# Kernel tuning notes

Measured on AMD Instinct MI355X. Metric: run time of the kernel, lower is better.

## Reference

```python
import jax, jax.numpy as jnp
import numpy as np
import math

N_HEADS = 12
EPS = 1e-5

def _layernorm(x, w, b):
    # torch .var() is unbiased (ddof=1)
    mean = jnp.mean(x, axis=-1, keepdims=True)
    var = jnp.var(x, axis=-1, keepdims=True, ddof=1)
    return (x - mean) / jnp.sqrt(var + EPS) * w + b

def _gelu_tanh(x):
    c = math.sqrt(2.0 / math.pi)
    return 0.5 * x * (1.0 + jnp.tanh(c * (x + 0.044715 * x * x * x)))

def setup_inputs() -> dict:
    key = jax.random.key(0)
    ks = jax.random.split(key, 6)
    B, T, C = 4, 2048, 768
    s = 0.02
    return {
        "x": jax.random.normal(ks[0], (B, T, C), jnp.float32),
        "ln1_w": jnp.ones((C,), jnp.float32),
        "ln1_b": jnp.zeros((C,), jnp.float32),
        "c_attn_w": jax.random.normal(ks[1], (C, 3 * C), jnp.float32) * s,
        "c_attn_b": jnp.zeros((3 * C,), jnp.float32),
        "c_proj_w": jax.random.normal(ks[2], (C, C), jnp.float32) * s,
        "c_proj_b": jnp.zeros((C,), jnp.float32),
        "ln2_w": jnp.ones((C,), jnp.float32),
        "ln2_b": jnp.zeros((C,), jnp.float32),
        "fc_w": jax.random.normal(ks[3], (C, 4 * C), jnp.float32) * s,
        "fc_b": jnp.zeros((4 * C,), jnp.float32),
        "mproj_w": jax.random.normal(ks[4], (4 * C, C), jnp.float32) * s,
        "mproj_b": jnp.zeros((C,), jnp.float32),
    }

def _attention(x, c_attn_w, c_attn_b, c_proj_w, c_proj_b):
    B, T, C = x.shape
    H = N_HEADS
    D = C // H
    qkv = x @ c_attn_w + c_attn_b  # [B,T,3C]
    q, k, v = jnp.split(qkv, 3, axis=-1)
    q = q.reshape(B, T, H, D).transpose(0, 2, 1, 3)  # [B,H,T,D]
    k = k.reshape(B, T, H, D).transpose(0, 2, 1, 3)
    v = v.reshape(B, T, H, D).transpose(0, 2, 1, 3)
    scores = jnp.einsum("bhqd,bhkd->bhqk", q, k) * (D ** -0.5)  # [B,H,T,T]
    causal = jnp.tril(jnp.ones((T, T), bool))
    scores = jnp.where(causal[None, None], scores, jnp.float32(-jnp.inf))
    attn = jax.nn.softmax(scores, axis=-1)
    out = jnp.einsum("bhqk,bhkd->bhqd", attn, v)  # [B,H,T,D]
    out = out.transpose(0, 2, 1, 3).reshape(B, T, C)
    return out @ c_proj_w + c_proj_b

def reference(x, ln1_w, ln1_b, c_attn_w, c_attn_b, c_proj_w, c_proj_b,
              ln2_w, ln2_b, fc_w, fc_b, mproj_w, mproj_b):
    x = x + _attention(_layernorm(x, ln1_w, ln1_b), c_attn_w, c_attn_b, c_proj_w, c_proj_b)
    h = _gelu_tanh(_layernorm(x, ln2_w, ln2_b) @ fc_w + fc_b)
    return x + h @ mproj_w + mproj_b
```

## Files before the change

### kernel.cpp

```cpp
#include <hip/hip_runtime.h>
#include <hip/hip_bf16.h>
#include <cstdint>

#define BF __hip_bfloat16

typedef __bf16 v8bf __attribute__((ext_vector_type(8)));
typedef float  v4f  __attribute__((ext_vector_type(4)));

__device__ __forceinline__ float tof(BF v) { return __bfloat162float(v); }
__device__ __forceinline__ BF    tob(float v) { return __float2bfloat16(v); }
__device__ __forceinline__ float ldf(float v) { return v; }
__device__ __forceinline__ float ldf(BF v) { return tof(v); }
__device__ __forceinline__ void stv(float* p, float v) { *p = v; }
__device__ __forceinline__ void stv(BF* p, float v) { *p = tob(v); }

__device__ __forceinline__ v4f mfma16(v8bf a, v8bf b, v4f c) {
  return __builtin_amdgcn_mfma_f32_16x16x32_bf16(a, b, c, 0, 0, 0);
}

__device__ __forceinline__ void async16(const BF* g, BF* l) {
  __builtin_amdgcn_global_load_lds((const __attribute__((address_space(1))) void*)g,
                                   (__attribute__((address_space(3))) void*)l, 16, 0, 0);
}

__global__ __launch_bounds__(256) void transpose_k(const float* __restrict__ in,
                                                   BF* __restrict__ out, int R, int C) {
  __shared__ BF t[64][65];
  int tid = threadIdx.x;
  int c0 = blockIdx.x * 64, r0 = blockIdx.y * 64;
#pragma unroll
  for (int i = 0; i < 16; ++i) {
    int idx = i * 256 + tid;
    int rr = idx >> 6, cc = idx & 63;
    t[rr][cc] = tob(in[(size_t)(r0 + rr) * C + c0 + cc]);
  }
  __syncthreads();
#pragma unroll
  for (int i = 0; i < 16; ++i) {
    int idx = i * 256 + tid;
    int rr = idx >> 6, cc = idx & 63;
    out[(size_t)(c0 + rr) * R + r0 + cc] = t[cc][rr];
  }
}

__global__ __launch_bounds__(256) void prep_k(
    const float* __restrict__ caw, BF* __restrict__ oca,
    const float* __restrict__ pw,  BF* __restrict__ opj,
    const float* __restrict__ fw,  BF* __restrict__ ofc,
    const float* __restrict__ mw,  BF* __restrict__ omp,
    const float* __restrict__ x, const float* __restrict__ lw,
    const float* __restrict__ lb, BF* __restrict__ y) {
  __shared__ BF t[64][65];
  __shared__ float rs[4][2];
  const int bid = blockIdx.x;
  const int tid = threadIdx.x;
  if (bid < 1728) {
    const float* in; BF* out; int R, C, bx, by;
    if (bid < 432)       { in = caw; out = oca; R = 768;  C = 2304; bx = bid % 36; by = bid / 36; }
    else if (bid < 576)  { int i = bid - 432;  in = pw; out = opj; R = 768;  C = 768;  bx = i % 12; by = i / 12; }
    else if (bid < 1152) { int i = bid - 576;  in = fw; out = ofc; R = 768;  C = 3072; bx = i % 48; by = i / 48; }
    else                 { int i = bid - 1152; in = mw; out = omp; R = 3072; C = 768;  bx = i % 12; by = i / 12; }
    int c0 = bx * 64, r0 = by * 64;
#pragma unroll
    for (int i = 0; i < 16; ++i) {
      int idx = i * 256 + tid;
      int rr = idx >> 6, cc = idx & 63;
      t[rr][cc] = tob(in[(size_t)(r0 + rr) * C + c0 + cc]);
    }
    __syncthreads();
#pragma unroll
    for (int i = 0; i < 16; ++i) {
      int idx = i * 256 + tid;
      int rr = idx >> 6, cc = idx & 63;
      out[(size_t)(c0 + rr) * R + r0 + cc] = t[cc][rr];
    }
  } else {
    int row = bid - 1728;
    const float* xr = x + (size_t)row * 768;
    float v0 = xr[tid], v1 = xr[tid + 256], v2 = xr[tid + 512];
    float s1 = v0 + v1 + v2;
    float s2 = v0 * v0 + v1 * v1 + v2 * v2;
#pragma unroll
    for (int m = 32; m; m >>= 1) { s1 += __shfl_xor(s1, m); s2 += __shfl_xor(s2, m); }
    int wv = tid >> 6;
    if ((tid & 63) == 0) { rs[wv][0] = s1; rs[wv][1] = s2; }
    __syncthreads();
    s1 = rs[0][0] + rs[1][0] + rs[2][0] + rs[3][0];
    s2 = rs[0][1] + rs[1][1] + rs[2][1] + rs[3][1];
    float mean = s1 * (1.0f / 768.0f);
    float var = fmaxf((s2 - s1 * mean) * (1.0f / 767.0f), 0.0f);
    float rstd = rsqrtf(var + 1e-5f);
    BF* yr = y + (size_t)row * 768;
    yr[tid]       = tob((v0 - mean) * rstd * lw[tid]       + lb[tid]);
    yr[tid + 256] = tob((v1 - mean) * rstd * lw[tid + 256] + lb[tid + 256]);
    yr[tid + 512] = tob((v2 - mean) * rstd * lw[tid + 512] + lb[tid + 512]);
  }
}

__global__ __launch_bounds__(256) void vtrans_k(const BF* __restrict__ qkv,
                                                BF* __restrict__ vT) {
  __shared__ BF t[64][65];
  int tid = threadIdx.x;
  int t0 = blockIdx.x * 64;
  int bh = blockIdx.y;
  int b = bh / 12, h = bh % 12;
  const BF* src = qkv + (size_t)(b * 2048 + t0) * 2304 + 1536 + h * 64;
#pragma unroll
  for (int i = 0; i < 16; ++i) {
    int idx = i * 256 + tid;
    int rr = idx >> 6, cc = idx & 63;
    t[rr][cc] = src[(size_t)rr * 2304 + cc];
  }
  __syncthreads();
  BF* dst = vT + (size_t)bh * 64 * 2048 + t0;
#pragma unroll
  for (int i = 0; i < 16; ++i) {
    int idx = i * 256 + tid;
    int rr = idx >> 6, cc = idx & 63;
    dst[(size_t)rr * 2048 + cc] = t[cc][rr];
  }
}

template <typename TX>
__global__ __launch_bounds__(256) void ln_k(const TX* __restrict__ x,
                                            const float* __restrict__ w,
                                            const float* __restrict__ bia,
                                            BF* __restrict__ y) {
  int row = blockIdx.x, tid = threadIdx.x;
  const TX* xr = x + (size_t)row * 768;
  float v0 = ldf(xr[tid]), v1 = ldf(xr[tid + 256]), v2 = ldf(xr[tid + 512]);
  float s1 = v0 + v1 + v2;
  float s2 = v0 * v0 + v1 * v1 + v2 * v2;
#pragma unroll
  for (int m = 32; m; m >>= 1) { s1 += __shfl_xor(s1, m); s2 += __shfl_xor(s2, m); }
  __shared__ float rs[4][2];
  int wv = tid >> 6;
  if ((tid & 63) == 0) { rs[wv][0] = s1; rs[wv][1] = s2; }
  __syncthreads();
  s1 = rs[0][0] + rs[1][0] + rs[2][0] + rs[3][0];
  s2 = rs[0][1] + rs[1][1] + rs[2][1] + rs[3][1];
  float mean = s1 * (1.0f / 768.0f);
  float var = fmaxf((s2 - s1 * mean) * (1.0f / 767.0f), 0.0f);
  float rstd = rsqrtf(var + 1e-5f);
  BF* yr = y + (size_t)row * 768;
  yr[tid]       = tob((v0 - mean) * rstd * w[tid]       + bia[tid]);
  yr[tid + 256] = tob((v1 - mean) * rstd * w[tid + 256] + bia[tid + 256]);
  yr[tid + 512] = tob((v2 - mean) * rstd * w[tid + 512] + bia[tid + 512]);
}

__device__ __forceinline__ float gelu_f(float x) {
  float u = 0.7978845608028654f * (x + 0.044715f * x * x * x);
  float e = exp2f(2.8853900817779268f * u);
  return 0.5f * x * (1.0f + (1.0f - 2.0f / (e + 1.0f)));
}

template <int BN, int ACT, bool RESID, typename TR, typename TO>
__global__ __launch_bounds__(256) void gemm_sm_k(
    const BF* __restrict__ A, const BF* __restrict__ Bt, const float* __restrict__ bias,
    const TR* __restrict__ resid, TO* __restrict__ out, int M, int N, int K) {
  constexpr int NW = BN / 32;
  __shared__ __align__(16) BF As[2][128 * 64];
  __shared__ __align__(16) BF Bs[2][BN * 64];
  const int tid = threadIdx.x;
  const int w = tid >> 6, lane = tid & 63;
  const int quad = lane >> 4, l16 = lane & 15;
  const int gx = gridDim.x;
  const int nwg = gx * gridDim.y;
  const int lid = blockIdx.y * gx + blockIdx.x;
  const int swz = (lid & 7) * (nwg >> 3) + (lid >> 3);
  const int m0 = (swz / gx) * 128, n0 = (swz % gx) * BN;
  const int wm = (w >> 1) * 64, wn = (w & 1) * (BN / 2);
  const int sr = lane >> 3;
  const int sc = ((lane & 7) ^ sr) * 8;

  v4f acc[4][NW];
#pragma unroll
  for (int i = 0; i < 4; ++i)
#pragma unroll
    for (int j = 0; j < NW; ++j) acc[i][j] = (v4f){0.f, 0.f, 0.f, 0.f};

  auto stage = [&](int bsel, int k0) {
#pragma unroll
    for (int i = 0; i < 4; ++i) {
      int r0 = w * 32 + i * 8;
      async16(A + (size_t)(m0 + r0 + sr) * K + k0 + sc, &As[bsel][r0 * 64]);
    }
    if (BN == 128) {
#pragma unroll
      for (int i = 0; i < 4; ++i) {
        int r0 = w * 32 + i * 8;
        async16(Bt + (size_t)(n0 + r0 + sr) * K + k0 + sc, &Bs[bsel][r0 * 64]);
      }
    } else {
#pragma unroll
      for (int i = 0; i < 2; ++i) {
        int r0 = w * 16 + i * 8;
        async16(Bt + (size_t)(n0 + r0 + sr) * K + k0 + sc, &Bs[bsel][r0 * 64]);
      }
    }
  };

  const int nkt = K >> 6;
  stage(0, 0);
  __syncthreads();
  for (int kt = 0; kt < nkt; ++kt) {
    const int cur = kt & 1;
    if (kt + 1 < nkt) stage(cur ^ 1, (kt + 1) << 6);
#pragma unroll
    for (int kk = 0; kk < 2; ++kk) {
      v8bf af[4], bfv[NW];
#pragma unroll
      for (int mi = 0; mi < 4; ++mi) {
        int row = wm + mi * 16 + l16;
        af[mi] = *(const v8bf*)&As[cur][row * 64 + (((kk * 4 + quad) ^ (row & 7)) * 8)];
      }
#pragma unroll
      for (int nj = 0; nj < NW; ++nj) {
        int row = wn + nj * 16 + l16;
        bfv[nj] = *(const v8bf*)&Bs[cur][row * 64 + (((kk * 4 + quad) ^ (row & 7)) * 8)];
      }
      __builtin_amdgcn_s_setprio(1);
#pragma unroll
      for (int mi = 0; mi < 4; ++mi)
#pragma unroll
        for (int nj = 0; nj < NW; ++nj)
          acc[mi][nj] = mfma16(af[mi], bfv[nj], acc[mi][nj]);
      __builtin_amdgcn_s_setprio(0);
    }
    __syncthreads();
  }

#pragma unroll
  for (int nj = 0; nj < NW; ++nj) {
    int col = n0 + wn + nj * 16 + l16;
    float bv = bias[col];
#pragma unroll
    for (int mi = 0; mi < 4; ++mi) {
      v4f c = acc[mi][nj];
#pragma unroll
      for (int r = 0; r < 4; ++r) {
        int row = m0 + wm + mi * 16 + quad * 4 + r;
        float v = c[r] + bv;
        if (RESID) v += ldf(resid[(size_t)row * N + col]);
        if (ACT == 1) v = gelu_f(v);
        stv(&out[(size_t)row * N + col], v);
      }
    }
  }
}

template <int ACT, bool RESID, typename TR, typename TO>
__global__ __launch_bounds__(256) void gemm3_k(
    const BF* __restrict__ A, const BF* __restrict__ Bt, const float* __restrict__ bias,
    const TR* __restrict__ resid, TO* __restrict__ out, int M, int N, int K) {
  __shared__ __align__(16) BF As[3][128 * 64];
  __shared__ __align__(16) BF Bs[3][64 * 64];
  const int tid = threadIdx.x;
  const int w = tid >> 6, lane = tid & 63;
  const int quad = lane >> 4, l16 = lane & 15;
  const int gx = gridDim.x;
  const int nwg = gx * gridDim.y;
  const int lid = blockIdx.y * gx + blockIdx.x;
  const int swz = (lid & 7) * (nwg >> 3) + (lid >> 3);
  const int m0 = (swz / gx) * 128, n0 = (swz % gx) * 64;
  const int wm = (w >> 1) * 64, wn = (w & 1) * 32;
  const int sr = lane >> 3;
  const int sc = ((lane & 7) ^ sr) * 8;

  v4f acc[4][2];
#pragma unroll
  for (int i = 0; i < 4; ++i)
#pragma unroll
    for (int j = 0; j < 2; ++j) acc[i][j] = (v4f){0.f, 0.f, 0.f, 0.f};

  auto stage = [&](int bsel, int kt) {
    const int k0 = kt << 6;
#pragma unroll
    for (int i = 0; i < 4; ++i) {
      int r0 = w * 32 + i * 8;
      async16(A + (size_t)(m0 + r0 + sr) * K + k0 + sc, &As[bsel][r0 * 64]);
    }
#pragma unroll
    for (int i = 0; i < 2; ++i) {
      int r0 = w * 16 + i * 8;
      async16(Bt + (size_t)(n0 + r0 + sr) * K + k0 + sc, &Bs[bsel][r0 * 64]);
    }
  };

  const int nkt = K >> 6;
  stage(0, 0);
  stage(1, 1);
  asm volatile("s_waitcnt vmcnt(6)" ::: "memory");
  __builtin_amdgcn_s_barrier();
  asm volatile("" ::: "memory");

  for (int kt = 0; kt < nkt; ++kt) {
    if (kt + 2 < nkt) stage((kt + 2) % 3, kt + 2);
    const BF* Ab = As[kt % 3];
    const BF* Bb = Bs[kt % 3];
#pragma unroll
    for (int kk = 0; kk < 2; ++kk) {
      v8bf af[4], bfv[2];
#pragma unroll
      for (int mi = 0; mi < 4; ++mi) {
        int row = wm + mi * 16 + l16;
        af[mi] = *(const v8bf*)&Ab[row * 64 + (((kk * 4 + quad) ^ (row & 7)) * 8)];
      }
#pragma unroll
      for (int nj = 0; nj < 2; ++nj) {
        int row = wn + nj * 16 + l16;
        bfv[nj] = *(const v8bf*)&Bb[row * 64 + (((kk * 4 + quad) ^ (row & 7)) * 8)];
      }
      __builtin_amdgcn_s_setprio(1);
#pragma unroll
      for (int mi = 0; mi < 4; ++mi)
#pragma unroll
        for (int nj = 0; nj < 2; ++nj)
          acc[mi][nj] = mfma16(af[mi], bfv[nj], acc[mi][nj]);
      __builtin_amdgcn_s_setprio(0);
    }
    if (kt + 1 < nkt) {
      if (kt + 2 < nkt) asm volatile("s_waitcnt vmcnt(6)" ::: "memory");
      else              asm volatile("s_waitcnt vmcnt(0)" ::: "memory");
      __builtin_amdgcn_s_barrier();
      asm volatile("" ::: "memory");
    }
  }

#pragma unroll
  for (int nj = 0; nj < 2; ++nj) {
    int col = n0 + wn + nj * 16 + l16;
    float bv = bias[col];
#pragma unroll
    for (int mi = 0; mi < 4; ++mi) {
      v4f c = acc[mi][nj];
#pragma unroll
      for (int r = 0; r < 4; ++r) {
        int row = m0 + wm + mi * 16 + quad * 4 + r;
        float v = c[r] + bv;
        if (RESID) v += ldf(resid[(size_t)row * N + col]);
        if (ACT == 1) v = gelu_f(v);
        stv(&out[(size_t)row * N + col], v);
      }
    }
  }
}

__global__ __launch_bounds__(256) void attn_k(const BF* __restrict__ qkv,
                                              const BF* __restrict__ vT,
                                              BF* __restrict__ out) {
  __shared__ __align__(16) BF Ks[64 * 64];
  __shared__ __align__(16) BF Vs[64 * 64];
  __shared__ __align__(16) BF Ps[4][16 * 64];
  const int tid = threadIdx.x;
  const int w = tid >> 6, lane = tid & 63;
  const int quad = lane >> 4, l16 = lane & 15;
  const int bid = blockIdx.x;
  const int qi = 31 - (bid / 48);
  const int bh = bid % 48;
  const int b = bh / 12, h = bh % 12;
  const int q0 = qi * 64;
  const int qf = q0 + w * 16;
  BF* Pw = &Ps[w][0];
  const float L2E = 1.4426950408889634f;

  auto sz = [](int r, int c) { return (r << 6) + (c ^ ((r & 7) << 3)); };

  const BF* qp = qkv + (size_t)(b * 2048 + qf + l16) * 2304 + h * 64;
  v8bf q0v = *(const v8bf*)(qp + quad * 8);
  v8bf q1v = *(const v8bf*)(qp + 32 + quad * 8);
#pragma unroll
  for (int i = 0; i < 8; ++i) {
    q0v[i] = (__bf16)(tof((BF)q0v[i]) * 0.125f);
    q1v[i] = (__bf16)(tof((BF)q1v[i]) * 0.125f);
  }
  v8bf ones;
#pragma unroll
  for (int i = 0; i < 8; ++i) ones[i] = (__bf16)1.0f;

  v4f O[4], S;
#pragma unroll
  for (int j = 0; j < 4; ++j) O[j] = (v4f){0.f, 0.f, 0.f, 0.f};
  S = (v4f){0.f, 0.f, 0.f, 0.f};

  const BF* kg = qkv + (size_t)b * 2048 * 2304 + 768 + h * 64;
  const BF* vg = vT + (size_t)bh * 64 * 2048;
  const int r0 = tid >> 3, c0 = (tid & 7) * 8;
  const int r1 = r0 + 32;
  const int nIter = qi + 1;

  v8bf nk0 = *(const v8bf*)(kg + (size_t)r0 * 2304 + c0);
  v8bf nk1 = *(const v8bf*)(kg + (size_t)r1 * 2304 + c0);
  v8bf nv0 = *(const v8bf*)(vg + (size_t)r0 * 2048 + c0);
  v8bf nv1 = *(const v8bf*)(vg + (size_t)r1 * 2048 + c0);

  for (int t = 0; t < nIter; ++t) {
    const int kt0 = t * 64;
    __syncthreads();
    *(v8bf*)&Ks[sz(r0, c0)] = nk0;
    *(v8bf*)&Ks[sz(r1, c0)] = nk1;
    *(v8bf*)&Vs[sz(r0, c0)] = nv0;
    *(v8bf*)&Vs[sz(r1, c0)] = nv1;
    __syncthreads();
    if (t + 1 < nIter) {
      const int kn = kt0 + 64;
      nk0 = *(const v8bf*)(kg + (size_t)(kn + r0) * 2304 + c0);
      nk1 = *(const v8bf*)(kg + (size_t)(kn + r1) * 2304 + c0);
      nv0 = *(const v8bf*)(vg + (size_t)r0 * 2048 + kn + c0);
      nv1 = *(const v8bf*)(vg + (size_t)r1 * 2048 + kn + c0);
    }
    v4f s[4];
    __builtin_amdgcn_s_setprio(1);
#pragma unroll
    for (int nt = 0; nt < 4; ++nt) {
      v8bf kf0 = *(const v8bf*)&Ks[sz(nt * 16 + l16, quad * 8)];
      v8bf kf1 = *(const v8bf*)&Ks[sz(nt * 16 + l16, 32 + quad * 8)];
      s[nt] = mfma16(q1v, kf1, mfma16(q0v, kf0, (v4f){0.f, 0.f, 0.f, 0.f}));
    }
    __builtin_amdgcn_s_setprio(0);
    if (t < qi) {
#pragma unroll
      for (int nt = 0; nt < 4; ++nt)
#pragma unroll
        for (int r = 0; r < 4; ++r)
          Pw[sz(quad * 4 + r, nt * 16 + l16)] = tob(exp2f(s[nt][r] * L2E));
    } else {
#pragma unroll
      for (int nt = 0; nt < 4; ++nt) {
        int key = kt0 + nt * 16 + l16;
#pragma unroll
        for (int r = 0; r < 4; ++r) {
          int qrow = qf + quad * 4 + r;
          float p = (key <= qrow) ? exp2f(s[nt][r] * L2E) : 0.f;
          Pw[sz(quad * 4 + r, nt * 16 + l16)] = tob(p);
        }
      }
    }
    asm volatile("s_waitcnt lgkmcnt(0)" ::: "memory");
    v8bf p0 = *(const v8bf*)&Pw[sz(l16, quad * 8)];
    v8bf p1 = *(const v8bf*)&Pw[sz(l16, 32 + quad * 8)];
    __builtin_amdgcn_s_setprio(1);
#pragma unroll
    for (int j = 0; j < 4; ++j) {
      v8bf vf0 = *(const v8bf*)&Vs[sz(j * 16 + l16, quad * 8)];
      v8bf vf1 = *(const v8bf*)&Vs[sz(j * 16 + l16, 32 + quad * 8)];
      O[j] = mfma16(p1, vf1, mfma16(p0, vf0, O[j]));
    }
    S = mfma16(p1, ones, mfma16(p0, ones, S));
    __builtin_amdgcn_s_setprio(0);
  }

#pragma unroll
  for (int r = 0; r < 4; ++r) {
    float inv = 1.0f / S[r];
    int row = b * 2048 + qf + quad * 4 + r;
    BF* op = out + (size_t)row * 768 + h * 64 + l16;
#pragma unroll
    for (int j = 0; j < 4; ++j) op[j * 16] = tob(O[j][r] * inv);
  }
}

extern "C" void kernel_launch(void* const* d_in, const int* in_sizes, int n_in,
                              void* d_out, int out_size, void* d_ws, size_t ws_size,
                              hipStream_t stream) {
  const float* x        = (const float*)d_in[0];
  const float* ln1_w    = (const float*)d_in[1];
  const float* ln1_b    = (const float*)d_in[2];
  const float* c_attn_w = (const float*)d_in[3];
  const float* c_attn_b = (const float*)d_in[4];
  const float* c_proj_w = (const float*)d_in[5];
  const float* c_proj_b = (const float*)d_in[6];
  const float* ln2_w    = (const float*)d_in[7];
  const float* ln2_b    = (const float*)d_in[8];
  const float* fc_w     = (const float*)d_in[9];
  const float* fc_b     = (const float*)d_in[10];
  const float* mproj_w  = (const float*)d_in[11];
  const float* mproj_b  = (const float*)d_in[12];
  float* out = (float*)d_out;
  char* wsb = (char*)d_ws;
  dim3 blk(256);

  BF* vT = (BF*)((char*)d_out + 12582912);

  const size_t NEED_BIG = 89653248;
  if (ws_size >= NEED_BIG) {
    BF* qkv      = (BF*)(wsb);
    BF* hbuf     = (BF*)(wsb);
    BF* x2       = (BF*)(wsb + 50331648);
    BF* wT_attn  = (BF*)(wsb + 62914560);
    BF* wT_proj  = (BF*)(wsb + 66453504);
    BF* wT_fc    = (BF*)(wsb + 67633152);
    BF* wT_mproj = (BF*)(wsb + 72351744);
    BF* lnbuf    = (BF*)(wsb + 77070336);
    BF* attnout  = (BF*)d_out;

    prep_k<<<dim3(9920), blk, 0, stream>>>(c_attn_w, wT_attn, c_proj_w, wT_proj,
                                           fc_w, wT_fc, mproj_w, wT_mproj,
                                           x, ln1_w, ln1_b, lnbuf);
    gemm3_k<0, false, float, BF><<<dim3(36, 64), blk, 0, stream>>>(
        lnbuf, wT_attn, c_attn_b, (const float*)nullptr, qkv, 8192, 2304, 768);
    vtrans_k<<<dim3(32, 48), blk, 0, stream>>>(qkv, vT);
    attn_k<<<dim3(1536), blk, 0, stream>>>(qkv, vT, attnout);
    gemm3_k<0, true, float, BF><<<dim3(12, 64), blk, 0, stream>>>(
        attnout, wT_proj, c_proj_b, x, x2, 8192, 768, 768);
    ln_k<BF><<<8192, blk, 0, stream>>>(x2, ln2_w, ln2_b, lnbuf);
    gemm_sm_k<128, 1, false, float, BF><<<dim3(24, 64), blk, 0, stream>>>(
        lnbuf, wT_fc, fc_b, (const float*)nullptr, hbuf, 8192, 3072, 768);
    gemm3_k<0, true, BF, float><<<dim3(12, 64), blk, 0, stream>>>(
        hbuf, wT_mproj, mproj_b, x2, out, 8192, 768, 3072);
  } else {
    BF* ws       = (BF*)d_ws;
    BF* qkv      = ws;
    BF* attnout  = ws + (size_t)18874368;
    BF* wT_attn  = attnout;
    BF* x2       = ws;
    BF* wT_proj  = ws + (size_t)6291456;
    BF* wT_fc    = ws + (size_t)6881280;
    BF* wT_mproj = ws + (size_t)9240576;
    BF* hbuf     = ws + (size_t)11599872;
    BF* lnbuf    = (BF*)d_out;

    transpose_k<<<dim3(36, 12), blk, 0, stream>>>(c_attn_w, wT_attn, 768, 2304);
    ln_k<float><<<8192, blk, 0, stream>>>(x, ln1_w, ln1_b, lnbuf);
    gemm3_k<0, false, float, BF><<<dim3(36, 64), blk, 0, stream>>>(
        lnbuf, wT_attn, c_attn_b, (const float*)nullptr, qkv, 8192, 2304, 768);
    vtrans_k<<<dim3(32, 48), blk, 0, stream>>>(qkv, vT);
    attn_k<<<dim3(1536), blk, 0, stream>>>(qkv, vT, attnout);
    transpose_k<<<dim3(12, 12), blk, 0, stream>>>(c_proj_w, wT_proj, 768, 768);
    gemm3_k<0, true, float, BF><<<dim3(12, 64), blk, 0, stream>>>(
        attnout, wT_proj, c_proj_b, x, x2, 8192, 768, 768);
    ln_k<BF><<<8192, blk, 0, stream>>>(x2, ln2_w, ln2_b, lnbuf);
    transpose_k<<<dim3(48, 12), blk, 0, stream>>>(fc_w, wT_fc, 768, 3072);
    transpose_k<<<dim3(12, 48), blk, 0, stream>>>(mproj_w, wT_mproj, 3072, 768);
    for (int half = 1; half >= 0; --half) {
      size_t r0 = (size_t)half * 4096;
      gemm_sm_k<128, 1, false, float, BF><<<dim3(24, 32), blk, 0, stream>>>(
          lnbuf + r0 * 768, wT_fc, fc_b, (const float*)nullptr, hbuf, 4096, 3072, 768);
      gemm3_k<0, true, BF, float><<<dim3(12, 32), blk, 0, stream>>>(
          hbuf, wT_mproj, mproj_b, x2 + r0 * 768, out + r0 * 768, 4096, 768, 3072);
    }
  }
}
```

Measured before the change: 416.1 us.

## Replace triple-buffered GEMM with 64x128 double-buffered tile and revert to gemm_sm_k

Converts the 128x64 triple-buffered gemm3_k into a 64x128 double-buffered gemm64_k that synchronises with plain __syncthreads, and uses it for the FC GEMM. The QKV, attention-projection and MLP-projection GEMMs go back to the older gemm_sm_k variants with different tile widths. The aim is to trade tile shapes and pipelining depth per GEMM for better occupancy or wave count. The cost is a shallower prefetch pipeline and heavier barrier sync in the new kernel, which could expose global-load latency.

After: 359.7 us. -13.5%, faster.

```diff
diff --git a/kernel.cpp b/kernel.cpp
--- a/kernel.cpp
+++ b/kernel.cpp
@@ -250,11 +250,11 @@
 }
 
 template <int ACT, bool RESID, typename TR, typename TO>
-__global__ __launch_bounds__(256) void gemm3_k(
+__global__ __launch_bounds__(256) void gemm64_k(
     const BF* __restrict__ A, const BF* __restrict__ Bt, const float* __restrict__ bias,
     const TR* __restrict__ resid, TO* __restrict__ out, int M, int N, int K) {
-  __shared__ __align__(16) BF As[3][128 * 64];
-  __shared__ __align__(16) BF Bs[3][64 * 64];
+  __shared__ __align__(16) BF As[2][64 * 64];
+  __shared__ __align__(16) BF Bs[2][128 * 64];
   const int tid = threadIdx.x;
   const int w = tid >> 6, lane = tid & 63;
   const int quad = lane >> 4, l16 = lane & 15;
@@ -262,77 +262,66 @@
   const int nwg = gx * gridDim.y;
   const int lid = blockIdx.y * gx + blockIdx.x;
   const int swz = (lid & 7) * (nwg >> 3) + (lid >> 3);
-  const int m0 = (swz / gx) * 128, n0 = (swz % gx) * 64;
-  const int wm = (w >> 1) * 64, wn = (w & 1) * 32;
+  const int m0 = (swz / gx) * 64, n0 = (swz % gx) * 128;
+  const int wm = (w >> 1) * 32, wn = (w & 1) * 64;
   const int sr = lane >> 3;
   const int sc = ((lane & 7) ^ sr) * 8;
 
-  v4f acc[4][2];
-#pragma unroll
-  for (int i = 0; i < 4; ++i)
-#pragma unroll
-    for (int j = 0; j < 2; ++j) acc[i][j] = (v4f){0.f, 0.f, 0.f, 0.f};
-
-  auto stage = [&](int bsel, int kt) {
-    const int k0 = kt << 6;
+  v4f acc[2][4];
+#pragma unroll
+  for (int i = 0; i < 2; ++i)
+#pragma unroll
+    for (int j = 0; j < 4; ++j) acc[i][j] = (v4f){0.f, 0.f, 0.f, 0.f};
+
+  auto stage = [&](int bsel, int k0) {
+#pragma unroll
+    for (int i = 0; i < 2; ++i) {
+      int r0 = w * 16 + i * 8;
+      async16(A + (size_t)(m0 + r0 + sr) * K + k0 + sc, &As[bsel][r0 * 64]);
+    }
 #pragma unroll
     for (int i = 0; i < 4; ++i) {
       int r0 = w * 32 + i * 8;
-      async16(A + (size_t)(m0 + r0 + sr) * K + k0 + sc, &As[bsel][r0 * 64]);
-    }
-#pragma unroll
-    for (int i = 0; i < 2; ++i) {
-      int r0 = w * 16 + i * 8;
       async16(Bt + (size_t)(n0 + r0 + sr) * K + k0 + sc, &Bs[bsel][r0 * 64]);
     }
   };
 
   const int nkt = K >> 6;
   stage(0, 0);
-  stage(1, 1);
-  asm volatile("s_waitcnt vmcnt(6)" ::: "memory");
-  __builtin_amdgcn_s_barrier();
-  asm volatile("" ::: "memory");
-
+  __syncthreads();
   for (int kt = 0; kt < nkt; ++kt) {
-    if (kt + 2 < nkt) stage((kt + 2) % 3, kt + 2);
-    const BF* Ab = As[kt % 3];
-    const BF* Bb = Bs[kt % 3];
+    const int cur = kt & 1;
+    if (kt + 1 < nkt) stage(cur ^ 1, (kt + 1) << 6);
 #pragma unroll
     for (int kk = 0; kk < 2; ++kk) {
-      v8bf af[4], bfv[2];
-#pragma unroll
-      for (int mi = 0; mi < 4; ++mi) {
+      v8bf af[2], bfv[4];
+#pragma unroll
+      for (int mi = 0; mi < 2; ++mi) {
         int row = wm + mi * 16 + l16;
-        af[mi] = *(const v8bf*)&Ab[row * 64 + (((kk * 4 + quad) ^ (row & 7)) * 8)];
-      }
-#pragma unroll
-      for (int nj = 0; nj < 2; ++nj) {
+        af[mi] = *(const v8bf*)&As[cur][row * 64 + (((kk * 4 + quad) ^ (row & 7)) * 8)];
+      }
+#pragma unroll
+      for (int nj = 0; nj < 4; ++nj) {
         int row = wn + nj * 16 + l16;
-        bfv[nj] = *(const v8bf*)&Bb[row * 64 + (((kk * 4 + quad) ^ (row & 7)) * 8)];
+        bfv[nj] = *(const v8bf*)&Bs[cur][row * 64 + (((kk * 4 + quad) ^ (row & 7)) * 8)];
       }
       __builtin_amdgcn_s_setprio(1);
 #pragma unroll
-      for (int mi = 0; mi < 4; ++mi)
-#pragma unroll
-        for (int nj = 0; nj < 2; ++nj)
+      for (int mi = 0; mi < 2; ++mi)
+#pragma unroll
+        for (int nj = 0; nj < 4; ++nj)
           acc[mi][nj] = mfma16(af[mi], bfv[nj], acc[mi][nj]);
       __builtin_amdgcn_s_setprio(0);
     }
-    if (kt + 1 < nkt) {
-      if (kt + 2 < nkt) asm volatile("s_waitcnt vmcnt(6)" ::: "memory");
-      else              asm volatile("s_waitcnt vmcnt(0)" ::: "memory");
-      __builtin_amdgcn_s_barrier();
-      asm volatile("" ::: "memory");
-    }
-  }
-
-#pragma unroll
-  for (int nj = 0; nj < 2; ++nj) {
+    __syncthreads();
+  }
+
+#pragma unroll
+  for (int nj = 0; nj < 4; ++nj) {
     int col = n0 + wn + nj * 16 + l16;
     float bv = bias[col];
 #pragma unroll
-    for (int mi = 0; mi < 4; ++mi) {
+    for (int mi = 0; mi < 2; ++mi) {
       v4f c = acc[mi][nj];
 #pragma unroll
       for (int r = 0; r < 4; ++r) {
@@ -497,16 +486,16 @@
     prep_k<<<dim3(9920), blk, 0, stream>>>(c_attn_w, wT_attn, c_proj_w, wT_proj,
                                            fc_w, wT_fc, mproj_w, wT_mproj,
                                            x, ln1_w, ln1_b, lnbuf);
-    gemm3_k<0, false, float, BF><<<dim3(36, 64), blk, 0, stream>>>(
+    gemm_sm_k<128, 0, false, float, BF><<<dim3(18, 64), blk, 0, stream>>>(
         lnbuf, wT_attn, c_attn_b, (const float*)nullptr, qkv, 8192, 2304, 768);
     vtrans_k<<<dim3(32, 48), blk, 0, stream>>>(qkv, vT);
     attn_k<<<dim3(1536), blk, 0, stream>>>(qkv, vT, attnout);
-    gemm3_k<0, true, float, BF><<<dim3(12, 64), blk, 0, stream>>>(
+    gemm_sm_k<64, 0, true, float, BF><<<dim3(12, 64), blk, 0, stream>>>(
         attnout, wT_proj, c_proj_b, x, x2, 8192, 768, 768);
     ln_k<BF><<<8192, blk, 0, stream>>>(x2, ln2_w, ln2_b, lnbuf);
-    gemm_sm_k<128, 1, false, float, BF><<<dim3(24, 64), blk, 0, stream>>>(
+    gemm64_k<1, false, float, BF><<<dim3(24, 128), blk, 0, stream>>>(
         lnbuf, wT_fc, fc_b, (const float*)nullptr, hbuf, 8192, 3072, 768);
-    gemm3_k<0, true, BF, float><<<dim3(12, 64), blk, 0, stream>>>(
+    gemm_sm_k<64, 0, true, BF, float><<<dim3(12, 64), blk, 0, stream>>>(
         hbuf, wT_mproj, mproj_b, x2, out, 8192, 768, 3072);
   } else {
     BF* ws       = (BF*)d_ws;
@@ -522,12 +511,12 @@
 
     transpose_k<<<dim3(36, 12), blk, 0, stream>>>(c_attn_w, wT_attn, 768, 2304);
     ln_k<float><<<8192, blk, 0, stream>>>(x, ln1_w, ln1_b, lnbuf);
-    gemm3_k<0, false, float, BF><<<dim3(36, 64), blk, 0, stream>>>(
+    gemm_sm_k<128, 0, false, float, BF><<<dim3(18, 64), blk, 0, stream>>>(
         lnbuf, wT_attn, c_attn_b, (const float*)nullptr, qkv, 8192, 2304, 768);
     vtrans_k<<<dim3(32, 48), blk, 0, stream>>>(qkv, vT);
     attn_k<<<dim3(1536), blk, 0, stream>>>(qkv, vT, attnout);
     transpose_k<<<dim3(12, 12), blk, 0, stream>>>(c_proj_w, wT_proj, 768, 768);
-    gemm3_k<0, true, float, BF><<<dim3(12, 64), blk, 0, stream>>>(
+    gemm_sm_k<64, 0, true, float, BF><<<dim3(12, 64), blk, 0, stream>>>(
         attnout, wT_proj, c_proj_b, x, x2, 8192, 768, 768);
     ln_k<BF><<<8192, blk, 0, stream>>>(x2, ln2_w, ln2_b, lnbuf);
     transpose_k<<<dim3(48, 12), blk, 0, stream>>>(fc_w, wT_fc, 768, 3072);
@@ -536,7 +525,7 @@
       size_t r0 = (size_t)half * 4096;
       gemm_sm_k<128, 1, false, float, BF><<<dim3(24, 32), blk, 0, stream>>>(
           lnbuf + r0 * 768, wT_fc, fc_b, (const float*)nullptr, hbuf, 4096, 3072, 768);
-      gemm3_k<0, true, BF, float><<<dim3(12, 32), blk, 0, stream>>>(
+      gemm_sm_k<64, 0, true, BF, float><<<dim3(12, 32), blk, 0, stream>>>(
           hbuf, wT_mproj, mproj_b, x2 + r0 * 768, out + r0 * 768, 4096, 768, 3072);
     }
   }
```
